# Kernel tuning notes

Measured on AMD Instinct MI355X. Metric: run time of the kernel, lower is better.

## Reference

```python
import jax, jax.numpy as jnp
import numpy as np

B, S, HID, NH, FF, K = 2, 2048, 1024, 16, 4096, 512
DH = HID // NH


def setup_inputs() -> dict:
    key = jax.random.key(0)
    ks = jax.random.split(key, 24)
    w = lambda k, shape: (jax.random.normal(k, shape, jnp.float32) * 0.02)
    inp = {
        'x': jax.random.normal(ks[0], (B, S, HID), jnp.float32),
        'mask': jnp.ones((B, 1, 1, S), jnp.int32),
        'Wq': w(ks[1], (HID, HID)), 'bq': jnp.zeros((HID,), jnp.float32),
        'Wk': w(ks[2], (HID, HID)), 'bk': jnp.zeros((HID,), jnp.float32),
        'Wv': w(ks[3], (HID, HID)), 'bv': jnp.zeros((HID,), jnp.float32),
        'Wo': w(ks[4], (HID, HID)), 'bo': jnp.zeros((HID,), jnp.float32),
        'rel_emb': w(ks[5], (2 * K, HID)),
        'Wpk': w(ks[6], (HID, HID)), 'bpk': jnp.zeros((HID,), jnp.float32),
        'Wpq': w(ks[7], (HID, HID)), 'bpq': jnp.zeros((HID,), jnp.float32),
        'ln1_g': jnp.ones((HID,), jnp.float32), 'ln1_b': jnp.zeros((HID,), jnp.float32),
        'ln2_g': jnp.ones((HID,), jnp.float32), 'ln2_b': jnp.zeros((HID,), jnp.float32),
        'W1': w(ks[8], (HID, FF)), 'b1': jnp.zeros((FF,), jnp.float32),
        'W2': w(ks[9], (FF, HID)), 'b2': jnp.zeros((HID,), jnp.float32),
    }
    return inp


def _layernorm(x, g, b, eps=1e-6):
    m = jnp.mean(x, -1, keepdims=True)
    v = jnp.mean(jnp.square(x - m), -1, keepdims=True)
    return (x - m) * jax.lax.rsqrt(v + eps) * g + b


def _disentangled_attention(x, mask, Wq, bq, Wk, bk, Wv, bv, Wo, bo,
                            rel_emb, Wpk, bpk, Wpq, bpq):
    # content projections -> [B, NH, S, DH]
    def heads(t):
        return t.reshape(B, S, NH, DH).transpose(0, 2, 1, 3)
    q = heads(x @ Wq + bq)
    k = heads(x @ Wk + bk)
    v = heads(x @ Wv + bv)

    # relative position index: rel[i, j] = clip(i - j, -K, K-1) + K in [0, 2K)
    pos = jnp.arange(S)
    rel = jnp.clip(pos[:, None] - pos[None, :], -K, K - 1) + K  # [S, S]

    # projected relative-position embeddings -> [2K, NH, DH]
    pos_k = (rel_emb @ Wpk + bpk).reshape(2 * K, NH, DH)
    pos_q = (rel_emb @ Wpq + bpq).reshape(2 * K, NH, DH)

    # content-to-content
    c2c = jnp.einsum('bhid,bhjd->bhij', q, k)
    # content-to-position: gather over relative bucket per (i, j)
    c2p_att = jnp.einsum('bhid,rhd->bhir', q, pos_k)               # [B,NH,S,2K]
    c2p = jnp.take_along_axis(c2p_att, rel[None, None, :, :], axis=-1)
    # position-to-content: K_j . Q_r[delta(j, i)], gather then transpose
    p2c_att = jnp.einsum('bhjd,rhd->bhjr', k, pos_q)               # [B,NH,S,2K]
    p2c = jnp.take_along_axis(p2c_att, rel[None, None, :, :], axis=-1)
    p2c = p2c.transpose(0, 1, 3, 2)

    scale = 1.0 / jnp.sqrt(jnp.asarray(3 * DH, jnp.float32))
    scores = (c2c + c2p + p2c) * scale                             # [B,NH,S,S]
    scores = jnp.where(mask == 0, jnp.asarray(-1e9, scores.dtype), scores)
    attn = jax.nn.softmax(scores, axis=-1)

    out = jnp.einsum('bhij,bhjd->bhid', attn, v)
    out = out.transpose(0, 2, 1, 3).reshape(B, S, HID)
    return out @ Wo + bo


def reference(x, mask, Wq, bq, Wk, bk, Wv, bv, Wo, bo, rel_emb, Wpk, bpk,
              Wpq, bpq, ln1_g, ln1_b, ln2_g, ln2_b, W1, b1, W2, b2):
    # pre-norm sublayer 1: x + attn(LN(x))
    h = x + _disentangled_attention(_layernorm(x, ln1_g, ln1_b), mask,
                                    Wq, bq, Wk, bk, Wv, bv, Wo, bo,
                                    rel_emb, Wpk, bpk, Wpq, bpq)
    # pre-norm sublayer 2: h + FFN(LN(h)), GELU activation
    hn = _layernorm(h, ln2_g, ln2_b)
    ff = jax.nn.gelu(hn @ W1 + b1) @ W2 + b2
    return h + ff
```

## Files before the change

kernel.cpp:

```cpp
#include <hip/hip_runtime.h>
#include <cstdint>
#include <cstddef>

#define DEV __device__ __forceinline__

typedef __attribute__((ext_vector_type(4))) float  f32x4;
typedef __attribute__((ext_vector_type(4))) float  float4v;
typedef __attribute__((ext_vector_type(8))) short  s16x8;
typedef __attribute__((ext_vector_type(4))) short  s16x4;

static constexpr int BB = 2, SS = 2048, HIDN = 1024, NHH = 16, FFN = 4096, DH = 64;
static constexpr int TWOK = 1024;
static constexpr int HG = 8;
static constexpr float ATT_SCALE = 0.07216878364870322f;

DEV short f2bf(float f) {
  union { float f; uint32_t u; } v; v.f = f;
  uint32_t r = (v.u + 0x7fffu + ((v.u >> 16) & 1u)) >> 16;
  return (short)r;
}
DEV float bfu(unsigned short u) {
  union { uint32_t u; float f; } v; v.u = ((uint32_t)u) << 16; return v.f;
}
DEV int imin(int a, int b) { return a < b ? a : b; }
DEV int imax(int a, int b) { return a > b ? a : b; }

DEV void gl_lds16(const void* g, void* l) {
  __builtin_amdgcn_global_load_lds((const __attribute__((address_space(1))) void*)g,
                                   (__attribute__((address_space(3))) void*)l, 16, 0, 0);
}

#define MFMA16(a, b, c) __builtin_amdgcn_mfma_f32_16x16x32_bf16((a), (b), (c), 0, 0, 0)

__global__ __launch_bounds__(256) void k_tcast(const float* __restrict__ in,
                                               short* __restrict__ out, int R, int C) {
  __shared__ float t[32][33];
  const int bx = blockIdx.x * 32, by = blockIdx.y * 32;
  const int tx = threadIdx.x & 31, ty = threadIdx.x >> 5;
#pragma unroll
  for (int r = ty; r < 32; r += 8) t[r][tx] = in[(size_t)(by + r) * C + bx + tx];
  __syncthreads();
#pragma unroll
  for (int c = ty; c < 32; c += 8) out[(size_t)(bx + c) * R + by + tx] = f2bf(t[tx][c]);
}

struct TCBatch { const float* in[5]; short* out[5]; };
__global__ __launch_bounds__(256) void k_tcast5(TCBatch tc) {
  __shared__ float t[32][33];
  const float* in = tc.in[blockIdx.z];
  short* out = tc.out[blockIdx.z];
  const int bx = blockIdx.x * 32, by = blockIdx.y * 32;
  const int tx = threadIdx.x & 31, ty = threadIdx.x >> 5;
#pragma unroll
  for (int r = ty; r < 32; r += 8) t[r][tx] = in[(size_t)(by + r) * 1024 + bx + tx];
  __syncthreads();
#pragma unroll
  for (int c = ty; c < 32; c += 8) out[(size_t)(bx + c) * 1024 + by + tx] = f2bf(t[tx][c]);
}

__global__ __launch_bounds__(256) void k_cast(const float* __restrict__ in,
                                              short* __restrict__ out, int n4) {
  const int i = blockIdx.x * 256 + threadIdx.x;
  if (i < n4) {
    float4v v = ((const float4v*)in)[i];
    s16x4 o; o[0] = f2bf(v.x); o[1] = f2bf(v.y); o[2] = f2bf(v.z); o[3] = f2bf(v.w);
    ((s16x4*)out)[i] = o;
  }
}

__global__ __launch_bounds__(256) void k_ln(const float* __restrict__ x,
                                            const float* __restrict__ gw,
                                            const float* __restrict__ bw,
                                            short* __restrict__ out) {
  const int row = blockIdx.x, t = threadIdx.x, lane = t & 63, wv = t >> 6;
  __shared__ float red[8];
  const float4v v = ((const float4v*)(x + (size_t)row * HIDN))[t];
  float s = v.x + v.y + v.z + v.w;
#pragma unroll
  for (int d = 1; d < 64; d <<= 1) s += __shfl_xor(s, d, 64);
  if (lane == 0) red[wv] = s;
  __syncthreads();
  const float mean = (red[0] + red[1] + red[2] + red[3]) * (1.f / 1024.f);
  const float dx = v.x - mean, dy = v.y - mean, dz = v.z - mean, dw = v.w - mean;
  float s2 = dx * dx + dy * dy + dz * dz + dw * dw;
#pragma unroll
  for (int d = 1; d < 64; d <<= 1) s2 += __shfl_xor(s2, d, 64);
  if (lane == 0) red[4 + wv] = s2;
  __syncthreads();
  const float var = (red[4] + red[5] + red[6] + red[7]) * (1.f / 1024.f);
  const float rs = rsqrtf(var + 1e-6f);
  const float4v g4 = ((const float4v*)gw)[t], b4 = ((const float4v*)bw)[t];
  s16x4 o;
  o[0] = f2bf(dx * rs * g4.x + b4.x);
  o[1] = f2bf(dy * rs * g4.y + b4.y);
  o[2] = f2bf(dz * rs * g4.z + b4.z);
  o[3] = f2bf(dw * rs * g4.w + b4.w);
  ((s16x4*)(out + (size_t)row * HIDN))[t] = o;
}

DEV void gemm_main(const short* __restrict__ A, const short* __restrict__ Bt, int K,
                   int m0, int n0, int tid, int wm, int wn, int lr, int lg,
                   short* As, short* Bs, f32x4 acc[4][4]) {
  for (int k0 = 0; k0 < K; k0 += 32) {
#pragma unroll
    for (int c = tid; c < 512; c += 256) {
      const int row = c >> 2, col = (c & 3) * 8;
      gl_lds16(A + (size_t)(m0 + row) * K + k0 + col, (char*)As + c * 16);
      gl_lds16(Bt + (size_t)(n0 + row) * K + k0 + col, (char*)Bs + c * 16);
    }
    __syncthreads();
    s16x8 af[4], bf[4];
#pragma unroll
    for (int fi = 0; fi < 4; ++fi) af[fi] = *(const s16x8*)&As[(wm + fi * 16 + lr) * 32 + lg * 8];
#pragma unroll
    for (int fj = 0; fj < 4; ++fj) bf[fj] = *(const s16x8*)&Bs[(wn + fj * 16 + lr) * 32 + lg * 8];
#pragma unroll
    for (int fi = 0; fi < 4; ++fi)
#pragma unroll
      for (int fj = 0; fj < 4; ++fj) acc[fi][fj] = MFMA16(af[fi], bf[fj], acc[fi][fj]);
    __syncthreads();
  }
}

enum { OM_GELU = 0, OM_RESID = 1 };

template <int OM>
__global__ __launch_bounds__(256) void k_gemm(const short* __restrict__ A,
                                              const short* __restrict__ Bt,
                                              const float* __restrict__ bias,
                                              const float* __restrict__ resid,
                                              void* __restrict__ out,
                                              int M, int N, int K) {
  __shared__ short As[128 * 32];
  __shared__ short Bs[128 * 32];
  const int tid = threadIdx.x, lane = tid & 63, wave = tid >> 6;
  const int m0 = blockIdx.y * 128, n0 = blockIdx.x * 128;
  const int wm = (wave >> 1) * 64, wn = (wave & 1) * 64;
  const int lr = lane & 15, lg = lane >> 4;

  f32x4 acc[4][4];
#pragma unroll
  for (int i = 0; i < 4; ++i)
#pragma unroll
    for (int j = 0; j < 4; ++j) acc[i][j] = (f32x4){0.f, 0.f, 0.f, 0.f};
  gemm_main(A, Bt, K, m0, n0, tid, wm, wn, lr, lg, As, Bs, acc);

#pragma unroll
  for (int fi = 0; fi < 4; ++fi)
#pragma unroll
    for (int fj = 0; fj < 4; ++fj) {
      const int n = n0 + wn + fj * 16 + lr;
      const float bv = bias[n];
#pragma unroll
      for (int r = 0; r < 4; ++r) {
        const int m = m0 + wm + fi * 16 + lg * 4 + r;
        float v = acc[fi][fj][r] + bv;
        if constexpr (OM == OM_GELU) {
          const float z = 0.7978845608028654f * (v + 0.044715f * v * v * v);
          const float th = 1.f - 2.f / (1.f + __expf(2.f * z));
          ((short*)out)[(size_t)m * N + n] = f2bf(0.5f * v * (1.f + th));
        } else {
          ((float*)out)[(size_t)m * N + n] = v + resid[(size_t)m * N + n];
        }
      }
    }
}

__global__ __launch_bounds__(256) void k_gemm_qkv(const short* __restrict__ A,
                                                  const short* __restrict__ Bt,
                                                  const float* __restrict__ bq,
                                                  const float* __restrict__ bk,
                                                  const float* __restrict__ bv,
                                                  short* __restrict__ qo,
                                                  short* __restrict__ ko,
                                                  short* __restrict__ vo) {
  __shared__ short As[128 * 32];
  __shared__ short Bs[128 * 32];
  const int tid = threadIdx.x, lane = tid & 63, wave = tid >> 6;
  const int m0 = blockIdx.y * 128, n0 = blockIdx.x * 128;
  const int wm = (wave >> 1) * 64, wn = (wave & 1) * 64;
  const int lr = lane & 15, lg = lane >> 4;

  f32x4 acc[4][4];
#pragma unroll
  for (int i = 0; i < 4; ++i)
#pragma unroll
    for (int j = 0; j < 4; ++j) acc[i][j] = (f32x4){0.f, 0.f, 0.f, 0.f};
  gemm_main(A, Bt, 1024, m0, n0, tid, wm, wn, lr, lg, As, Bs, acc);

#pragma unroll
  for (int fi = 0; fi < 4; ++fi)
#pragma unroll
    for (int fj = 0; fj < 4; ++fj) {
      const int n = n0 + wn + fj * 16 + lr;
      const int proj = n >> 10, nn = n & 1023;
      const int hh = nn >> 6, dd = nn & 63;
      const float bvv = (proj == 0 ? bq : proj == 1 ? bk : bv)[nn];
#pragma unroll
      for (int r = 0; r < 4; ++r) {
        const int m = m0 + wm + fi * 16 + lg * 4 + r;
        const int b = m >> 11, s = m & (SS - 1);
        const float v = acc[fi][fj][r] + bvv;
        if (proj == 2)
          vo[(((size_t)b * NHH + hh) * DH + dd) * SS + s] = f2bf(v);
        else
          (proj == 0 ? qo : ko)[(((size_t)b * NHH + hh) * SS + s) * DH + dd] = f2bf(v);
      }
    }
}

__global__ __launch_bounds__(256) void k_gemm_pos(const short* __restrict__ A,
                                                  const short* __restrict__ Bt,
                                                  const float* __restrict__ bpk,
                                                  const float* __restrict__ bpq,
                                                  short* __restrict__ pko,
                                                  short* __restrict__ pqo) {
  __shared__ short As[128 * 32];
  __shared__ short Bs[128 * 32];
  const int tid = threadIdx.x, lane = tid & 63, wave = tid >> 6;
  const int m0 = blockIdx.y * 128, n0 = blockIdx.x * 128;
  const int wm = (wave >> 1) * 64, wn = (wave & 1) * 64;
  const int lr = lane & 15, lg = lane >> 4;

  f32x4 acc[4][4];
#pragma unroll
  for (int i = 0; i < 4; ++i)
#pragma unroll
    for (int j = 0; j < 4; ++j) acc[i][j] = (f32x4){0.f, 0.f, 0.f, 0.f};
  gemm_main(A, Bt, 1024, m0, n0, tid, wm, wn, lr, lg, As, Bs, acc);

#pragma unroll
  for (int fi = 0; fi < 4; ++fi)
#pragma unroll
    for (int fj = 0; fj < 4; ++fj) {
      const int n = n0 + wn + fj * 16 + lr;
      const int pos = n >> 10, nn = n & 1023;
      const int hh = nn >> 6, dd = nn & 63;
      const float bvv = (pos == 0 ? bpk : bpq)[nn];
      short* ob = pos == 0 ? pko : pqo;
#pragma unroll
      for (int r = 0; r < 4; ++r) {
        const int m = m0 + wm + fi * 16 + lg * 4 + r;
        ob[((size_t)hh * TWOK + m) * DH + dd] = f2bf(acc[fi][fj][r] + bvv);
      }
    }
}

__global__ __launch_bounds__(256) void k_posgemm(const short* __restrict__ qh,
                                                 const short* __restrict__ kh,
                                                 const short* __restrict__ posk,
                                                 const short* __restrict__ posq,
                                                 short* __restrict__ c2pO,
                                                 short* __restrict__ p2cO,
                                                 short* __restrict__ p2cE, int h0) {
  __shared__ short As[128 * 64];
  __shared__ short Bs[128 * 64];
  const int tid = threadIdx.x, lane = tid & 63, wave = tid >> 6;
  const int z = blockIdx.z;
  const int hl = z & (HG - 1), b = (z >> 3) & 1, isP = z >> 4;
  const int h = h0 + hl;
  const int bhl = b * HG + hl;
  const int m0 = blockIdx.y * 128, n0 = blockIdx.x * 128;
  const int wm = (wave >> 1) * 64, wn = (wave & 1) * 64;
  const int lr = lane & 15, lg = lane >> 4;
  const short* Ab = (isP ? kh : qh) + ((size_t)b * NHH + h) * SS * DH;
  const short* Pb = (isP ? posq : posk) + (size_t)h * TWOK * DH;
  short* ob = (isP ? p2cO : c2pO) + (size_t)bhl * SS * TWOK;

#pragma unroll
  for (int c = tid; c < 1024; c += 256) {
    const int row = c >> 3, col = (c & 7) * 8;
    gl_lds16(Ab + (size_t)(m0 + row) * DH + col, (char*)As + c * 16);
    gl_lds16(Pb + (size_t)(n0 + row) * DH + col, (char*)Bs + c * 16);
  }
  __syncthreads();

  f32x4 acc[4][4];
#pragma unroll
  for (int i = 0; i < 4; ++i)
#pragma unroll
    for (int j = 0; j < 4; ++j) acc[i][j] = (f32x4){0.f, 0.f, 0.f, 0.f};

#pragma unroll
  for (int ks = 0; ks < 2; ++ks) {
    s16x8 af[4], bf[4];
#pragma unroll
    for (int fi = 0; fi < 4; ++fi) af[fi] = *(const s16x8*)&As[(wm + fi * 16 + lr) * 64 + ks * 32 + lg * 8];
#pragma unroll
    for (int fj = 0; fj < 4; ++fj) bf[fj] = *(const s16x8*)&Bs[(wn + fj * 16 + lr) * 64 + ks * 32 + lg * 8];
#pragma unroll
    for (int fi = 0; fi < 4; ++fi)
#pragma unroll
      for (int fj = 0; fj < 4; ++fj) acc[fi][fj] = MFMA16(af[fi], bf[fj], acc[fi][fj]);
  }

#pragma unroll
  for (int fi = 0; fi < 4; ++fi)
#pragma unroll
    for (int fj = 0; fj < 4; ++fj) {
      const int n = n0 + wn + fj * 16 + lr;
#pragma unroll
      for (int r = 0; r < 4; ++r) {
        const int m = m0 + wm + fi * 16 + lg * 4 + r;
        const short val = f2bf(acc[fi][fj][r]);
        ob[(size_t)m * TWOK + n] = val;
        if (isP) {
          if (n == 0)        p2cE[((size_t)bhl * 2 + 0) * SS + m] = val;
          if (n == TWOK - 1) p2cE[((size_t)bhl * 2 + 1) * SS + m] = val;
        }
      }
    }
}

__global__ __launch_bounds__(256) void k_attn(const short* __restrict__ qh,
                                              const short* __restrict__ kh,
                                              const short* __restrict__ vT,
                                              const short* __restrict__ c2p,
                                              const short* __restrict__ p2c,
                                              const short* __restrict__ p2cE,
                                              const int* __restrict__ mask,
                                              short* __restrict__ ao, int h0) {
  __shared__ char smem[4 * 16 * 68 * 4];
  __shared__ float Mm[4][16];
  __shared__ float Lm[4][16];
  float (*Om)[16][68] = (float(*)[16][68])smem;
  short (*Ps)[16][72] = (short(*)[16][72])smem;

  const int tid = threadIdx.x, lane = tid & 63, wv = tid >> 6;
  const int lr = lane & 15, lg = lane >> 4;

  const int bid = blockIdx.x;
  const int itile = bid & 127;
  const int hl = (bid >> 7) & (HG - 1);
  const int b = bid >> 10;
  const int h = h0 + hl;
  const int i0 = itile * 16;
  const size_t bhoff = ((size_t)b * NHH + h) * SS * DH;
  const size_t bhl = (size_t)b * HG + hl;
  const int jq0 = wv * (SS / 4);

  const short* qrow = qh + bhoff + (size_t)(i0 + lr) * DH + lg * 8;
  const s16x8 qa0 = *(const s16x8*)qrow;
  const s16x8 qa1 = *(const s16x8*)(qrow + 32);

  const unsigned short* c2prow[4];
  float cLoV[4], cHiV[4];
#pragma unroll
  for (int r = 0; r < 4; ++r) {
    c2prow[r] = (const unsigned short*)(c2p + (bhl * SS + (size_t)(i0 + lg * 4 + r)) * TWOK);
    cLoV[r] = bfu(c2prow[r][0]);
    cHiV[r] = bfu(c2prow[r][TWOK - 1]);
  }
  const unsigned short* p2cb = (const unsigned short*)(p2c + bhl * SS * TWOK);
  const unsigned short* pE0 = (const unsigned short*)(p2cE + (bhl * 2 + 0) * SS);
  const unsigned short* pE1 = (const unsigned short*)(p2cE + (bhl * 2 + 1) * SS);

  const int dbase = i0 + lg * 4 - lr;

  f32x4 oacc[4];
  float mprev[4], lsum[4];
#pragma unroll
  for (int r = 0; r < 4; ++r) {
    mprev[r] = -1e30f; lsum[r] = 0.f; oacc[r] = (f32x4){0.f, 0.f, 0.f, 0.f};
  }

  for (int jt = 0; jt < SS / 4 / 64; ++jt) {
    const int j0 = jq0 + jt * 64;
    const int d0 = i0 - j0;

    f32x4 sacc[4];
#pragma unroll
    for (int fj = 0; fj < 4; ++fj) {
      const short* krow = kh + bhoff + (size_t)(j0 + fj * 16 + lr) * DH + lg * 8;
      const s16x8 k0 = *(const s16x8*)krow;
      const s16x8 k1 = *(const s16x8*)(krow + 32);
      f32x4 a = (f32x4){0.f, 0.f, 0.f, 0.f};
      a = MFMA16(qa0, k0, a);
      a = MFMA16(qa1, k1, a);
      sacc[fj] = a;
    }

    float pvv[4][4];
    if (d0 >= 576) {
#pragma unroll
      for (int fj = 0; fj < 4; ++fj) {
        const int jl = fj * 16 + lr;
        const bool ok = mask[(size_t)b * SS + j0 + jl] != 0;
        const float pe = bfu(pE0[j0 + jl]);
#pragma unroll
        for (int r = 0; r < 4; ++r) {
          const float s = (sacc[fj][r] + cHiV[r] + pe) * ATT_SCALE;
          pvv[fj][r] = ok ? s : -1e9f;
        }
      }
    } else if (d0 <= -528) {
#pragma unroll
      for (int fj = 0; fj < 4; ++fj) {
        const int jl = fj * 16 + lr;
        const bool ok = mask[(size_t)b * SS + j0 + jl] != 0;
        const float pe = bfu(pE1[j0 + jl]);
#pragma unroll
        for (int r = 0; r < 4; ++r) {
          const float s = (sacc[fj][r] + cLoV[r] + pe) * ATT_SCALE;
          pvv[fj][r] = ok ? s : -1e9f;
        }
      }
    } else {
#pragma unroll
      for (int fj = 0; fj < 4; ++fj) {
        const int jl = fj * 16 + lr;
        const bool ok = mask[(size_t)b * SS + j0 + jl] != 0;
        const unsigned short* prow = p2cb + (size_t)(j0 + jl) * TWOK;
        const int dl0 = dbase - fj * 16 - j0;
#pragma unroll
        for (int r = 0; r < 4; ++r) {
          const int dl = dl0 + r;
          const int cc = imin(imax(dl + 512, 0), 1023);
          const int cp = imin(imax(512 - dl, 0), 1023);
          const float s = (sacc[fj][r] + bfu(c2prow[r][cc]) + bfu(prow[cp])) * ATT_SCALE;
          pvv[fj][r] = ok ? s : -1e9f;
        }
      }
    }

#pragma unroll
    for (int r = 0; r < 4; ++r) {
      float m = fmaxf(fmaxf(pvv[0][r], pvv[1][r]), fmaxf(pvv[2][r], pvv[3][r]));
#pragma unroll
      for (int dd = 1; dd < 16; dd <<= 1) m = fmaxf(m, __shfl_xor(m, dd, 64));
      const float mnew = fmaxf(mprev[r], m);
      const float corr = __expf(mprev[r] - mnew);
      float rs = 0.f;
#pragma unroll
      for (int fj = 0; fj < 4; ++fj) { pvv[fj][r] = __expf(pvv[fj][r] - mnew); rs += pvv[fj][r]; }
#pragma unroll
      for (int dd = 1; dd < 16; dd <<= 1) rs += __shfl_xor(rs, dd, 64);
      lsum[r] = lsum[r] * corr + rs;
      mprev[r] = mnew;
#pragma unroll
      for (int fd = 0; fd < 4; ++fd) oacc[fd][r] *= corr;
    }

#pragma unroll
    for (int fj = 0; fj < 4; ++fj)
#pragma unroll
      for (int r = 0; r < 4; ++r)
        Ps[wv][lg * 4 + r][fj * 16 + lr] = f2bf(pvv[fj][r]);

    const s16x8 pa0 = *(const s16x8*)&Ps[wv][lr][lg * 8];
    const s16x8 pa1 = *(const s16x8*)&Ps[wv][lr][32 + lg * 8];
#pragma unroll
    for (int fd = 0; fd < 4; ++fd) {
      const short* vrow = vT + bhoff + (size_t)(fd * 16 + lr) * SS + j0 + lg * 8;
      const s16x8 v0 = *(const s16x8*)vrow;
      const s16x8 v1 = *(const s16x8*)(vrow + 32);
      oacc[fd] = MFMA16(pa0, v0, oacc[fd]);
      oacc[fd] = MFMA16(pa1, v1, oacc[fd]);
    }
  }

  __syncthreads();
#pragma unroll
  for (int fd = 0; fd < 4; ++fd)
#pragma unroll
    for (int r = 0; r < 4; ++r)
      Om[wv][lg * 4 + r][fd * 16 + lr] = oacc[fd][r];
  if (lr == 0) {
#pragma unroll
    for (int r = 0; r < 4; ++r) { Mm[wv][lg * 4 + r] = mprev[r]; Lm[wv][lg * 4 + r] = lsum[r]; }
  }
  __syncthreads();

#pragma unroll
  for (int r = 0; r < 4; ++r) {
    const int il = lg * 4 + r;
    float mt = fmaxf(fmaxf(Mm[0][il], Mm[1][il]), fmaxf(Mm[2][il], Mm[3][il]));
    float L = 0.f, o = 0.f;
#pragma unroll
    for (int w = 0; w < 4; ++w) {
      const float sc = __expf(Mm[w][il] - mt);
      L += Lm[w][il] * sc;
      o += Om[w][il][wv * 16 + lr] * sc;
    }
    ao[((size_t)b * SS + i0 + il) * HIDN + h * DH + wv * 16 + lr] = f2bf(o / L);
  }
}

extern "C" void kernel_launch(void* const* d_in, const int* in_sizes, int n_in,
                              void* d_out, int out_size, void* d_ws, size_t ws_size,
                              hipStream_t stream) {
  const float* x   = (const float*)d_in[0];
  const int* mask  = (const int*)d_in[1];
  const float* Wq  = (const float*)d_in[2];  const float* bq  = (const float*)d_in[3];
  const float* Wk  = (const float*)d_in[4];  const float* bk  = (const float*)d_in[5];
  const float* Wv  = (const float*)d_in[6];  const float* bv  = (const float*)d_in[7];
  const float* Wo  = (const float*)d_in[8];  const float* bo  = (const float*)d_in[9];
  const float* rel = (const float*)d_in[10];
  const float* Wpk = (const float*)d_in[11]; const float* bpk = (const float*)d_in[12];
  const float* Wpq = (const float*)d_in[13]; const float* bpq = (const float*)d_in[14];
  const float* g1  = (const float*)d_in[15]; const float* be1 = (const float*)d_in[16];
  const float* g2  = (const float*)d_in[17]; const float* be2 = (const float*)d_in[18];
  const float* W1  = (const float*)d_in[19]; const float* bf1 = (const float*)d_in[20];
  const float* W2  = (const float*)d_in[21]; const float* bf2 = (const float*)d_in[22];
  float* out = (float*)d_out;

  char* ws = (char*)d_ws;
  const size_t MB = (size_t)1 << 20;
  short* aoB   = (short*)(ws + 0 * MB);
  short* qhB   = (short*)(ws + 8 * MB);
  short* khB   = (short*)(ws + 16 * MB);
  short* vTB   = (short*)(ws + 24 * MB);
  short* poskB = (short*)(ws + 32 * MB);
  short* posqB = (short*)(ws + 34 * MB);
  short* xn    = (short*)(ws + 36 * MB);
  short* WqT   = (short*)(ws + 44 * MB);
  short* WkT   = (short*)(ws + 46 * MB);
  short* WvT   = (short*)(ws + 48 * MB);
  short* WpkT  = (short*)(ws + 50 * MB);
  short* WpqT  = (short*)(ws + 52 * MB);
  short* relbf = (short*)(ws + 54 * MB);
  short* c2pG  = (short*)(ws + 36 * MB);
  short* p2cG  = (short*)(ws + 100 * MB);
  short* p2cE  = (short*)(ws + 164 * MB);
  short* WoT   = (short*)(ws + 36 * MB);
  short* hnB   = (short*)(ws + 38 * MB);
  short* W1T   = (short*)(ws + 46 * MB);
  short* W2T   = (short*)(ws + 54 * MB);
  short* midB  = (short*)(ws + 62 * MB);
  (void)ws_size; (void)in_sizes; (void)n_in; (void)out_size;

  const int M = BB * SS;

  TCBatch tc;
  tc.in[0] = Wq;  tc.out[0] = WqT;
  tc.in[1] = Wk;  tc.out[1] = WkT;
  tc.in[2] = Wv;  tc.out[2] = WvT;
  tc.in[3] = Wpk; tc.out[3] = WpkT;
  tc.in[4] = Wpq; tc.out[4] = WpqT;
  k_tcast5<<<dim3(32, 32, 5), 256, 0, stream>>>(tc);
  k_cast<<<1024, 256, 0, stream>>>(rel, relbf, 1024 * 1024 / 4);
  k_ln<<<M, 256, 0, stream>>>(x, g1, be1, xn);

  k_gemm_qkv<<<dim3(24, 32), 256, 0, stream>>>(xn, WqT, bq, bk, bv, qhB, khB, vTB);
  k_gemm_pos<<<dim3(16, 8), 256, 0, stream>>>(relbf, WpkT, bpk, bpq, poskB, posqB);

  for (int g = 0; g < NHH / HG; ++g) {
    const int h0 = g * HG;
    k_posgemm<<<dim3(8, 16, 4 * HG), 256, 0, stream>>>(qhB, khB, poskB, posqB,
                                                       c2pG, p2cG, p2cE, h0);
    k_attn<<<BB * HG * 128, 256, 0, stream>>>(qhB, khB, vTB, c2pG, p2cG, p2cE, mask, aoB, h0);
  }

  k_tcast<<<dim3(32, 32), 256, 0, stream>>>(Wo, WoT, 1024, 1024);
  k_gemm<OM_RESID><<<dim3(8, 32), 256, 0, stream>>>(aoB, WoT, bo, x, out, M, 1024, 1024);
  k_ln<<<M, 256, 0, stream>>>(out, g2, be2, hnB);
  k_tcast<<<dim3(128, 32), 256, 0, stream>>>(W1, W1T, 1024, 4096);
  k_tcast<<<dim3(32, 128), 256, 0, stream>>>(W2, W2T, 4096, 1024);
  k_gemm<OM_GELU><<<dim3(32, 32), 256, 0, stream>>>(hnB, W1T, bf1, nullptr, midB, M, 4096, 1024);
  k_gemm<OM_RESID><<<dim3(8, 32), 256, 0, stream>>>(midB, W2T, bf2, out, out, M, 1024, 4096);
}
```

Before: 680.5 us.

## Store p2c in diagonal layout and software-pipeline gathers in attention

```diff
diff --git a/kernel.cpp b/kernel.cpp
--- a/kernel.cpp
+++ b/kernel.cpp
@@ -251,10 +251,11 @@
                                                  const short* __restrict__ posk,
                                                  const short* __restrict__ posq,
                                                  short* __restrict__ c2pO,
-                                                 short* __restrict__ p2cO,
+                                                 short* __restrict__ p2cD,
                                                  short* __restrict__ p2cE, int h0) {
   __shared__ short As[128 * 64];
   __shared__ short Bs[128 * 64];
+  __shared__ short L[128 * 129];
   const int tid = threadIdx.x, lane = tid & 63, wave = tid >> 6;
   const int z = blockIdx.z;
   const int hl = z & (HG - 1), b = (z >> 3) & 1, isP = z >> 4;
@@ -265,7 +266,6 @@
   const int lr = lane & 15, lg = lane >> 4;
   const short* Ab = (isP ? kh : qh) + ((size_t)b * NHH + h) * SS * DH;
   const short* Pb = (isP ? posq : posk) + (size_t)h * TWOK * DH;
-  short* ob = (isP ? p2cO : c2pO) + (size_t)bhl * SS * TWOK;
 
 #pragma unroll
   for (int c = tid; c < 1024; c += 256) {
@@ -294,29 +294,63 @@
       for (int fj = 0; fj < 4; ++fj) acc[fi][fj] = MFMA16(af[fi], bf[fj], acc[fi][fj]);
   }
 
-#pragma unroll
-  for (int fi = 0; fi < 4; ++fi)
-#pragma unroll
-    for (int fj = 0; fj < 4; ++fj) {
-      const int n = n0 + wn + fj * 16 + lr;
-#pragma unroll
-      for (int r = 0; r < 4; ++r) {
-        const int m = m0 + wm + fi * 16 + lg * 4 + r;
-        const short val = f2bf(acc[fi][fj][r]);
-        ob[(size_t)m * TWOK + n] = val;
-        if (isP) {
+  if (!isP) {
+    short* ob = c2pO + (size_t)bhl * SS * TWOK;
+#pragma unroll
+    for (int fi = 0; fi < 4; ++fi)
+#pragma unroll
+      for (int fj = 0; fj < 4; ++fj) {
+        const int n = n0 + wn + fj * 16 + lr;
+#pragma unroll
+        for (int r = 0; r < 4; ++r) {
+          const int m = m0 + wm + fi * 16 + lg * 4 + r;
+          ob[(size_t)m * TWOK + n] = f2bf(acc[fi][fj][r]);
+        }
+      }
+  } else {
+#pragma unroll
+    for (int fi = 0; fi < 4; ++fi)
+#pragma unroll
+      for (int fj = 0; fj < 4; ++fj) {
+        const int n = n0 + wn + fj * 16 + lr;
+        const int nl = n - n0;
+#pragma unroll
+        for (int r = 0; r < 4; ++r) {
+          const int m = m0 + wm + fi * 16 + lg * 4 + r;
+          const int ml = m - m0;
+          const short val = f2bf(acc[fi][fj][r]);
+          L[ml * 129 + nl] = val;
           if (n == 0)        p2cE[((size_t)bhl * 2 + 0) * SS + m] = val;
           if (n == TWOK - 1) p2cE[((size_t)bhl * 2 + 1) * SS + m] = val;
         }
       }
-    }
-}
+    __syncthreads();
+    const int nl = tid & 127, ty = tid >> 7;
+    const int ibase = m0 - n0 + 385;
+    short* pD = p2cD + (size_t)bhl * SS * TWOK;
+    for (int p = 0; p < 128; ++p) {
+      const int il = p * 2 + ty;
+      if (il < 255) {
+        const int ml = nl + il - 127;
+        const int ig = ibase + il;
+        if (ml >= 0 && ml < 128 && ig >= 0 && ig < SS)
+          pD[(size_t)ig * TWOK + n0 + nl] = L[ml * 129 + nl];
+      }
+    }
+  }
+}
+
+struct GS {
+  uint32_t g[16];
+  uint32_t pe[4];
+  int mk[4];
+};
 
 __global__ __launch_bounds__(256) void k_attn(const short* __restrict__ qh,
                                               const short* __restrict__ kh,
                                               const short* __restrict__ vT,
                                               const short* __restrict__ c2p,
-                                              const short* __restrict__ p2c,
+                                              const short* __restrict__ p2cD,
                                               const short* __restrict__ p2cE,
                                               const int* __restrict__ mask,
                                               short* __restrict__ ao, int h0) {
@@ -351,7 +385,7 @@
     cLoV[r] = bfu(c2prow[r][0]);
     cHiV[r] = bfu(c2prow[r][TWOK - 1]);
   }
-  const unsigned short* p2cb = (const unsigned short*)(p2c + bhl * SS * TWOK);
+  const ptrdiff_t pdelta = (const char*)p2cD - (const char*)c2p;
   const unsigned short* pE0 = (const unsigned short*)(p2cE + (bhl * 2 + 0) * SS);
   const unsigned short* pE1 = (const unsigned short*)(p2cE + (bhl * 2 + 1) * SS);
 
@@ -364,7 +398,37 @@
     mprev[r] = -1e30f; lsum[r] = 0.f; oacc[r] = (f32x4){0.f, 0.f, 0.f, 0.f};
   }
 
-  for (int jt = 0; jt < SS / 4 / 64; ++jt) {
+  auto issueG = [&](int jt, GS& G) {
+    const int j0 = jq0 + jt * 64;
+    const int d0 = i0 - j0;
+#pragma unroll
+    for (int fj = 0; fj < 4; ++fj) G.mk[fj] = mask[(size_t)b * SS + j0 + fj * 16 + lr];
+    if (d0 >= 576) {
+#pragma unroll
+      for (int fj = 0; fj < 4; ++fj) G.g[fj] = pE0[j0 + fj * 16 + lr];
+    } else if (d0 <= -528) {
+#pragma unroll
+      for (int fj = 0; fj < 4; ++fj) G.g[fj] = pE1[j0 + fj * 16 + lr];
+    } else {
+#pragma unroll
+      for (int fj = 0; fj < 4; ++fj) {
+        const int j = j0 + fj * 16 + lr;
+        G.pe[fj] = (uint32_t)pE0[j] | ((uint32_t)pE1[j] << 16);
+        const int dl0 = dbase - fj * 16 - j0;
+#pragma unroll
+        for (int r = 0; r < 4; ++r) {
+          const int dl = dl0 + r;
+          const int cc = imin(imax(dl + 512, 0), 1023);
+          const int cp = imin(imax(512 - dl, 0), 1023);
+          const unsigned short* pDrow =
+              (const unsigned short*)((const char*)c2prow[r] + pdelta);
+          G.g[fj * 4 + r] = (uint32_t)c2prow[r][cc] | ((uint32_t)pDrow[cp] << 16);
+        }
+      }
+    }
+  };
+
+  auto tileCompute = [&](int jt, const GS& G) {
     const int j0 = jq0 + jt * 64;
     const int d0 = i0 - j0;
 
@@ -379,14 +443,20 @@
       a = MFMA16(qa1, k1, a);
       sacc[fj] = a;
     }
+    s16x8 vf0[4], vf1[4];
+#pragma unroll
+    for (int fd = 0; fd < 4; ++fd) {
+      const short* vrow = vT + bhoff + (size_t)(fd * 16 + lr) * SS + j0 + lg * 8;
+      vf0[fd] = *(const s16x8*)vrow;
+      vf1[fd] = *(const s16x8*)(vrow + 32);
+    }
 
     float pvv[4][4];
     if (d0 >= 576) {
 #pragma unroll
       for (int fj = 0; fj < 4; ++fj) {
-        const int jl = fj * 16 + lr;
-        const bool ok = mask[(size_t)b * SS + j0 + jl] != 0;
-        const float pe = bfu(pE0[j0 + jl]);
+        const bool ok = G.mk[fj] != 0;
+        const float pe = bfu((unsigned short)G.g[fj]);
 #pragma unroll
         for (int r = 0; r < 4; ++r) {
           const float s = (sacc[fj][r] + cHiV[r] + pe) * ATT_SCALE;
@@ -396,9 +466,8 @@
     } else if (d0 <= -528) {
 #pragma unroll
       for (int fj = 0; fj < 4; ++fj) {
-        const int jl = fj * 16 + lr;
-        const bool ok = mask[(size_t)b * SS + j0 + jl] != 0;
-        const float pe = bfu(pE1[j0 + jl]);
+        const bool ok = G.mk[fj] != 0;
+        const float pe = bfu((unsigned short)G.g[fj]);
 #pragma unroll
         for (int r = 0; r < 4; ++r) {
           const float s = (sacc[fj][r] + cLoV[r] + pe) * ATT_SCALE;
@@ -408,16 +477,18 @@
     } else {
 #pragma unroll
       for (int fj = 0; fj < 4; ++fj) {
-        const int jl = fj * 16 + lr;
-        const bool ok = mask[(size_t)b * SS + j0 + jl] != 0;
-        const unsigned short* prow = p2cb + (size_t)(j0 + jl) * TWOK;
+        const bool ok = G.mk[fj] != 0;
+        const float pe0 = bfu((unsigned short)(G.pe[fj] & 0xffffu));
+        const float pe1 = bfu((unsigned short)(G.pe[fj] >> 16));
         const int dl0 = dbase - fj * 16 - j0;
 #pragma unroll
         for (int r = 0; r < 4; ++r) {
-          const int dl = dl0 + r;
-          const int cc = imin(imax(dl + 512, 0), 1023);
-          const int cp = imin(imax(512 - dl, 0), 1023);
-          const float s = (sacc[fj][r] + bfu(c2prow[r][cc]) + bfu(prow[cp])) * ATT_SCALE;
+          const uint32_t g = G.g[fj * 4 + r];
+          const int raw = 512 - (dl0 + r);
+          float p2cv = bfu((unsigned short)(g >> 16));
+          p2cv = raw < 0 ? pe0 : p2cv;
+          p2cv = raw > 1023 ? pe1 : p2cv;
+          const float s = (sacc[fj][r] + bfu((unsigned short)(g & 0xffffu)) + p2cv) * ATT_SCALE;
           pvv[fj][r] = ok ? s : -1e9f;
         }
       }
@@ -451,12 +522,20 @@
     const s16x8 pa1 = *(const s16x8*)&Ps[wv][lr][32 + lg * 8];
 #pragma unroll
     for (int fd = 0; fd < 4; ++fd) {
-      const short* vrow = vT + bhoff + (size_t)(fd * 16 + lr) * SS + j0 + lg * 8;
-      const s16x8 v0 = *(const s16x8*)vrow;
-      const s16x8 v1 = *(const s16x8*)(vrow + 32);
-      oacc[fd] = MFMA16(pa0, v0, oacc[fd]);
-      oacc[fd] = MFMA16(pa1, v1, oacc[fd]);
-    }
+      oacc[fd] = MFMA16(pa0, vf0[fd], oacc[fd]);
+      oacc[fd] = MFMA16(pa1, vf1[fd], oacc[fd]);
+    }
+  };
+
+  GS gA, gB;
+  issueG(0, gA);
+#pragma unroll
+  for (int jt2 = 0; jt2 < 4; ++jt2) {
+    const int t0 = jt2 * 2, t1 = t0 + 1;
+    issueG(t1, gB);
+    tileCompute(t0, gA);
+    if (t1 < 7) issueG(t1 + 1, gA);
+    tileCompute(t1, gB);
   }
 
   __syncthreads();
@@ -520,7 +599,7 @@
   short* WpqT  = (short*)(ws + 52 * MB);
   short* relbf = (short*)(ws + 54 * MB);
   short* c2pG  = (short*)(ws + 36 * MB);
-  short* p2cG  = (short*)(ws + 100 * MB);
+  short* p2cDG = (short*)(ws + 100 * MB);
   short* p2cE  = (short*)(ws + 164 * MB);
   short* WoT   = (short*)(ws + 36 * MB);
   short* hnB   = (short*)(ws + 38 * MB);
@@ -547,8 +626,8 @@
   for (int g = 0; g < NHH / HG; ++g) {
     const int h0 = g * HG;
     k_posgemm<<<dim3(8, 16, 4 * HG), 256, 0, stream>>>(qhB, khB, poskB, posqB,
-                                                       c2pG, p2cG, p2cE, h0);
-    k_attn<<<BB * HG * 128, 256, 0, stream>>>(qhB, khB, vTB, c2pG, p2cG, p2cE, mask, aoB, h0);
+                                                       c2pG, p2cDG, p2cE, h0);
+    k_attn<<<BB * HG * 128, 256, 0, stream>>>(qhB, khB, vTB, c2pG, p2cDG, p2cE, mask, aoB, h0);
   }
 
   k_tcast<<<dim3(32, 32), 256, 0, stream>>>(Wo, WoT, 1024, 1024);
```

Result: slower. 818.5 us (+20.3%).

## Store p2c table diagonally re-indexed so attention reads it row-aligned like c2p

Applied to the files above, without the earlier changes.

```diff
diff --git a/kernel.cpp b/kernel.cpp
--- a/kernel.cpp
+++ b/kernel.cpp
@@ -251,10 +251,11 @@
                                                  const short* __restrict__ posk,
                                                  const short* __restrict__ posq,
                                                  short* __restrict__ c2pO,
-                                                 short* __restrict__ p2cO,
+                                                 short* __restrict__ p2cD,
                                                  short* __restrict__ p2cE, int h0) {
   __shared__ short As[128 * 64];
   __shared__ short Bs[128 * 64];
+  __shared__ short L[128 * 129];
   const int tid = threadIdx.x, lane = tid & 63, wave = tid >> 6;
   const int z = blockIdx.z;
   const int hl = z & (HG - 1), b = (z >> 3) & 1, isP = z >> 4;
@@ -265,7 +266,6 @@
   const int lr = lane & 15, lg = lane >> 4;
   const short* Ab = (isP ? kh : qh) + ((size_t)b * NHH + h) * SS * DH;
   const short* Pb = (isP ? posq : posk) + (size_t)h * TWOK * DH;
-  short* ob = (isP ? p2cO : c2pO) + (size_t)bhl * SS * TWOK;
 
 #pragma unroll
   for (int c = tid; c < 1024; c += 256) {
@@ -294,29 +294,57 @@
       for (int fj = 0; fj < 4; ++fj) acc[fi][fj] = MFMA16(af[fi], bf[fj], acc[fi][fj]);
   }
 
-#pragma unroll
-  for (int fi = 0; fi < 4; ++fi)
-#pragma unroll
-    for (int fj = 0; fj < 4; ++fj) {
-      const int n = n0 + wn + fj * 16 + lr;
-#pragma unroll
-      for (int r = 0; r < 4; ++r) {
-        const int m = m0 + wm + fi * 16 + lg * 4 + r;
-        const short val = f2bf(acc[fi][fj][r]);
-        ob[(size_t)m * TWOK + n] = val;
-        if (isP) {
+  if (!isP) {
+    short* ob = c2pO + (size_t)bhl * SS * TWOK;
+#pragma unroll
+    for (int fi = 0; fi < 4; ++fi)
+#pragma unroll
+      for (int fj = 0; fj < 4; ++fj) {
+        const int n = n0 + wn + fj * 16 + lr;
+#pragma unroll
+        for (int r = 0; r < 4; ++r) {
+          const int m = m0 + wm + fi * 16 + lg * 4 + r;
+          ob[(size_t)m * TWOK + n] = f2bf(acc[fi][fj][r]);
+        }
+      }
+  } else {
+#pragma unroll
+    for (int fi = 0; fi < 4; ++fi)
+#pragma unroll
+      for (int fj = 0; fj < 4; ++fj) {
+        const int n = n0 + wn + fj * 16 + lr;
+        const int nl = n - n0;
+#pragma unroll
+        for (int r = 0; r < 4; ++r) {
+          const int m = m0 + wm + fi * 16 + lg * 4 + r;
+          const int ml = m - m0;
+          const short val = f2bf(acc[fi][fj][r]);
+          L[ml * 129 + nl] = val;
           if (n == 0)        p2cE[((size_t)bhl * 2 + 0) * SS + m] = val;
           if (n == TWOK - 1) p2cE[((size_t)bhl * 2 + 1) * SS + m] = val;
         }
       }
-    }
+    __syncthreads();
+    const int nl = tid & 127, ty = tid >> 7;
+    const int ibase = m0 - n0 + 385;
+    short* pD = p2cD + (size_t)bhl * SS * TWOK;
+    for (int p = 0; p < 128; ++p) {
+      const int il = p * 2 + ty;
+      if (il < 255) {
+        const int ml = nl + il - 127;
+        const int ig = ibase + il;
+        if (ml >= 0 && ml < 128 && ig >= 0 && ig < SS)
+          pD[(size_t)ig * TWOK + n0 + nl] = L[ml * 129 + nl];
+      }
+    }
+  }
 }
 
 __global__ __launch_bounds__(256) void k_attn(const short* __restrict__ qh,
                                               const short* __restrict__ kh,
                                               const short* __restrict__ vT,
                                               const short* __restrict__ c2p,
-                                              const short* __restrict__ p2c,
+                                              const short* __restrict__ p2cD,
                                               const short* __restrict__ p2cE,
                                               const int* __restrict__ mask,
                                               short* __restrict__ ao, int h0) {
@@ -351,7 +379,7 @@
     cLoV[r] = bfu(c2prow[r][0]);
     cHiV[r] = bfu(c2prow[r][TWOK - 1]);
   }
-  const unsigned short* p2cb = (const unsigned short*)(p2c + bhl * SS * TWOK);
+  const ptrdiff_t pdelta = (const char*)p2cD - (const char*)c2p;
   const unsigned short* pE0 = (const unsigned short*)(p2cE + (bhl * 2 + 0) * SS);
   const unsigned short* pE1 = (const unsigned short*)(p2cE + (bhl * 2 + 1) * SS);
 
@@ -410,14 +438,21 @@
       for (int fj = 0; fj < 4; ++fj) {
         const int jl = fj * 16 + lr;
         const bool ok = mask[(size_t)b * SS + j0 + jl] != 0;
-        const unsigned short* prow = p2cb + (size_t)(j0 + jl) * TWOK;
+        const float pe0 = bfu(pE0[j0 + jl]);
+        const float pe1 = bfu(pE1[j0 + jl]);
         const int dl0 = dbase - fj * 16 - j0;
 #pragma unroll
         for (int r = 0; r < 4; ++r) {
           const int dl = dl0 + r;
           const int cc = imin(imax(dl + 512, 0), 1023);
-          const int cp = imin(imax(512 - dl, 0), 1023);
-          const float s = (sacc[fj][r] + bfu(c2prow[r][cc]) + bfu(prow[cp])) * ATT_SCALE;
+          const int raw = 512 - dl;
+          const int cp = imin(imax(raw, 0), 1023);
+          const unsigned short* pDrow =
+              (const unsigned short*)((const char*)c2prow[r] + pdelta);
+          float p2cv = bfu(pDrow[cp]);
+          p2cv = raw < 0 ? pe0 : p2cv;
+          p2cv = raw > 1023 ? pe1 : p2cv;
+          const float s = (sacc[fj][r] + bfu(c2prow[r][cc]) + p2cv) * ATT_SCALE;
           pvv[fj][r] = ok ? s : -1e9f;
         }
       }
@@ -520,7 +555,7 @@
   short* WpqT  = (short*)(ws + 52 * MB);
   short* relbf = (short*)(ws + 54 * MB);
   short* c2pG  = (short*)(ws + 36 * MB);
-  short* p2cG  = (short*)(ws + 100 * MB);
+  short* p2cDG = (short*)(ws + 100 * MB);
   short* p2cE  = (short*)(ws + 164 * MB);
   short* WoT   = (short*)(ws + 36 * MB);
   short* hnB   = (short*)(ws + 38 * MB);
@@ -547,8 +582,8 @@
   for (int g = 0; g < NHH / HG; ++g) {
     const int h0 = g * HG;
     k_posgemm<<<dim3(8, 16, 4 * HG), 256, 0, stream>>>(qhB, khB, poskB, posqB,
-                                                       c2pG, p2cG, p2cE, h0);
-    k_attn<<<BB * HG * 128, 256, 0, stream>>>(qhB, khB, vTB, c2pG, p2cG, p2cE, mask, aoB, h0);
+                                                       c2pG, p2cDG, p2cE, h0);
+    k_attn<<<BB * HG * 128, 256, 0, stream>>>(qhB, khB, vTB, c2pG, p2cDG, p2cE, mask, aoB, h0);
   }
 
   k_tcast<<<dim3(32, 32), 256, 0, stream>>>(Wo, WoT, 1024, 1024);
```

Result: slower. 723.2 us (+6.3%).
